# Performance work log

Measured on AMD Instinct MI355X. Metric: run time of the kernel, lower is better.

The kernel has to match this reference:

```python
import jax, jax.numpy as jnp
import numpy as np

B, S, D, H = 128, 1024, 128, 256
ODE_UNFOLDS = 6
EPS = 1e-8


def setup_inputs() -> dict:
    key = jax.random.key(0)
    ks = jax.random.split(key, 14)
    u = lambda k, shape, lo, hi: jax.random.uniform(k, shape, jnp.float32, lo, hi)
    # ncps LTCCell default init ranges; FullyConnected wiring => sparsity masks all ones,
    # erev entries are +/-1 polarities (prob 2/3 excitatory)
    return {
        "x": jax.random.normal(ks[0], (B, S, D), jnp.float32),
        "gleak": u(ks[1], (H,), 0.001, 1.0),
        "vleak": u(ks[2], (H,), -0.2, 0.2),
        "cm": u(ks[3], (H,), 0.4, 0.6),
        "w": u(ks[4], (H, H), 0.001, 1.0),
        "sigma": u(ks[5], (H, H), 3.0, 8.0),
        "mu": u(ks[6], (H, H), 0.3, 0.8),
        "erev": jax.random.bernoulli(ks[7], 2.0 / 3.0, (H, H)).astype(jnp.float32) * 2.0 - 1.0,
        "sensory_w": u(ks[8], (D, H), 0.001, 1.0),
        "sensory_sigma": u(ks[9], (D, H), 3.0, 8.0),
        "sensory_mu": u(ks[10], (D, H), 0.3, 0.8),
        "sensory_erev": jax.random.bernoulli(ks[11], 2.0 / 3.0, (D, H)).astype(jnp.float32) * 2.0 - 1.0,
        "input_w": jnp.ones((D,), jnp.float32),
        "input_b": jnp.zeros((D,), jnp.float32),
    }


def reference(x, gleak, vleak, cm, w, sigma, mu, erev,
              sensory_w, sensory_sigma, sensory_mu, sensory_erev,
              input_w, input_b):
    # NoiseLTC forward in eval mode (noise applied only when training).
    # implicit_param_constraints=True => softplus on gleak, cm, w, sensory_w.
    sp = jax.nn.softplus
    gleak_p = sp(gleak)                      # [H]
    cm_t = sp(cm) * ODE_UNFOLDS             # cm / (elapsed_time=1.0 / ode_unfolds)
    w_p = sp(w)                              # [H, H]
    sw_p = sp(sensory_w)                     # [D, H]

    def step(h, xt):
        xin = xt * input_w + input_b         # affine input mapping, [B, D]
        # sensory synapse activation: [B, D, H]
        s_act = sw_p * jax.nn.sigmoid(sensory_sigma * (xin[:, :, None] - sensory_mu))
        w_num_s = jnp.sum(s_act * sensory_erev, axis=1)  # [B, H]
        w_den_s = jnp.sum(s_act, axis=1)                 # [B, H]

        def unfold(v, _):
            w_act = w_p * jax.nn.sigmoid(sigma * (v[:, :, None] - mu))  # [B, H, H]
            w_num = jnp.sum(w_act * erev, axis=1) + w_num_s
            w_den = jnp.sum(w_act, axis=1) + w_den_s
            num = cm_t * v + gleak_p * vleak + w_num
            den = cm_t + gleak_p + w_den
            return num / (den + EPS), None

        v, _ = jax.lax.scan(unfold, h, None, length=ODE_UNFOLDS)
        # output_size == state_size, so output is the full new state
        return v, v

    h0 = jnp.zeros((x.shape[0], H), x.dtype)
    h_final, outs = jax.lax.scan(step, h0, jnp.swapaxes(x, 0, 1))  # outs: [S, B, H]
    readout = jnp.swapaxes(outs, 0, 1)                             # [B, S, H]
    return readout, h_final
```

## Files before the change

### kernel.cpp

```cpp
#include <hip/hip_runtime.h>
#include <hip/hip_bf16.h>

#define HN 256
#define DN 128
#define SL 1024
#define BN 128
#define NUNF 6

static __device__ __forceinline__ float fexp2(float x) { return __builtin_amdgcn_exp2f(x); }
static __device__ __forceinline__ float frcp(float x) { return __builtin_amdgcn_rcpf(x); }

__global__ void ltc_prep(const float* __restrict__ gleak, const float* __restrict__ vleak,
                         const float* __restrict__ cm,    const float* __restrict__ w,
                         const float* __restrict__ sigma, const float* __restrict__ mu,
                         const float* __restrict__ erev,
                         const float* __restrict__ sw,    const float* __restrict__ ssig,
                         const float* __restrict__ smu,   const float* __restrict__ serev,
                         const float* __restrict__ iw,    const float* __restrict__ ib,
                         float* __restrict__ ws)
{
    const float L2E = 1.44269504088896340736f;
    float* rp  = ws;
    float* spp = ws + 3 * HN * HN;
    float* hv  = ws + 3 * HN * HN + 3 * DN * HN;
    const int stride = gridDim.x * blockDim.x;
    const int tid0 = blockIdx.x * blockDim.x + threadIdx.x;

    for (int idx = tid0; idx < HN * HN; idx += stride) {
        float sg = sigma[idx];
        float wp = log1pf(expf(w[idx]));
        rp[3 * idx + 0] = -sg * L2E;
        rp[3 * idx + 1] = sg * mu[idx] * L2E;
        rp[3 * idx + 2] = wp * erev[idx];
    }
    for (int idx = tid0; idx < DN * HN; idx += stride) {
        int d = idx >> 8;
        float sg = ssig[idx];
        float wp = log1pf(expf(sw[idx]));
        spp[3 * idx + 0] = -sg * L2E * iw[d];
        spp[3 * idx + 1] = sg * (smu[idx] - ib[d]) * L2E;
        spp[3 * idx + 2] = wp * serev[idx];
    }
    if (tid0 < HN) {
        float gl = log1pf(expf(gleak[tid0]));
        float ct = log1pf(expf(cm[tid0])) * (float)NUNF;
        hv[tid0]          = gl * vleak[tid0];
        hv[HN + tid0]     = ct;
        hv[2 * HN + tid0] = ct + gl;
    }
}

__global__ __launch_bounds__(1024) void ltc_main(
    const float* __restrict__ x, const float* __restrict__ rp,
    const float* __restrict__ spp, const float* __restrict__ hv,
    float* __restrict__ out)
{
    const int b = blockIdx.x;
    const int tid = threadIdx.x;
    const int h = tid & (HN - 1);
    const int c = tid >> 8;

    __shared__ __align__(16) float v_[HN];
    __shared__ __align__(16) float xs[DN];
    __shared__ __align__(16) float sred[4][HN][2];

    float cmt = 0.f, gv = 0.f, dcn = 0.f;
    if (tid < HN) {
        gv  = hv[tid];
        cmt = hv[HN + tid];
        dcn = hv[2 * HN + tid];
        v_[tid] = 0.f;
    }
    __syncthreads();

    const float* xrow = x + (size_t)b * SL * DN;
    float* orow = out + (size_t)b * SL * HN;
    float wns = 0.f, wds = 0.f, vnew = 0.f;

    for (int t = 0; t < SL; ++t) {
        if (tid < DN) xs[tid] = xrow[(size_t)t * DN + tid];
        __syncthreads();

        {
            float sn = 0.f, sd = 0.f;
            const float* p = spp + (size_t)(c * 32 * HN + h) * 3;
            const float4* xv4 = reinterpret_cast<const float4*>(&xs[c * 32]);
            #pragma unroll 2
            for (int j = 0; j < 8; ++j) {
                float4 xv = xv4[j];
                #pragma unroll
                for (int q = 0; q < 4; ++q) {
                    float xq = (q == 0) ? xv.x : (q == 1) ? xv.y : (q == 2) ? xv.z : xv.w;
                    float pa = p[0], pb = p[1], pc = p[2];
                    float u = fexp2(fmaf(pa, xq, pb));
                    float r = frcp(1.0f + u);
                    sn = fmaf(pc, r, sn);
                    sd = fmaf(fabsf(pc), r, sd);
                    p += 3 * HN;
                }
            }
            sred[c][h][0] = sn;
            sred[c][h][1] = sd;
        }
        __syncthreads();
        if (tid < HN) {
            wns = sred[0][tid][0] + sred[1][tid][0] + sred[2][tid][0] + sred[3][tid][0];
            wds = sred[0][tid][1] + sred[1][tid][1] + sred[2][tid][1] + sred[3][tid][1];
        }
        __syncthreads();

        #pragma unroll 1
        for (int k = 0; k < NUNF; ++k) {
            float nm = 0.f, dn = 0.f;
            const float* p = rp + (size_t)(c * 64 * HN + h) * 3;
            const float4* v4 = reinterpret_cast<const float4*>(&v_[c * 64]);
            #pragma unroll 2
            for (int j = 0; j < 16; ++j) {
                float4 vv = v4[j];
                #pragma unroll
                for (int q = 0; q < 4; ++q) {
                    float vq = (q == 0) ? vv.x : (q == 1) ? vv.y : (q == 2) ? vv.z : vv.w;
                    float pa = p[0], pb = p[1], pc = p[2];
                    float u = fexp2(fmaf(pa, vq, pb));
                    float r = frcp(1.0f + u);
                    nm = fmaf(pc, r, nm);
                    dn = fmaf(fabsf(pc), r, dn);
                    p += 3 * HN;
                }
            }
            sred[c][h][0] = nm;
            sred[c][h][1] = dn;
            __syncthreads();
            if (tid < HN) {
                float num = sred[0][tid][0] + sred[1][tid][0] + sred[2][tid][0] + sred[3][tid][0] + wns;
                float den = sred[0][tid][1] + sred[1][tid][1] + sred[2][tid][1] + sred[3][tid][1] + wds;
                float vo = v_[tid];
                num = fmaf(cmt, vo, gv) + num;
                den = dcn + den + 1e-8f;
                vnew = num / den;
                v_[tid] = vnew;
            }
            __syncthreads();
        }

        if (tid < HN) orow[(size_t)t * HN + tid] = vnew;
    }
    if (tid < HN) out[(size_t)BN * SL * HN + (size_t)b * HN + tid] = vnew;
}

extern "C" void kernel_launch(void* const* d_in, const int* in_sizes, int n_in,
                              void* d_out, int out_size, void* d_ws, size_t ws_size,
                              hipStream_t stream) {
    const float* x     = (const float*)d_in[0];
    const float* gleak = (const float*)d_in[1];
    const float* vleak = (const float*)d_in[2];
    const float* cm    = (const float*)d_in[3];
    const float* w     = (const float*)d_in[4];
    const float* sigma = (const float*)d_in[5];
    const float* mu    = (const float*)d_in[6];
    const float* erev  = (const float*)d_in[7];
    const float* sw    = (const float*)d_in[8];
    const float* ssig  = (const float*)d_in[9];
    const float* smu   = (const float*)d_in[10];
    const float* serev = (const float*)d_in[11];
    const float* iw    = (const float*)d_in[12];
    const float* ib    = (const float*)d_in[13];

    float* ws = (float*)d_ws;

    ltc_prep<<<128, 256, 0, stream>>>(gleak, vleak, cm, w, sigma, mu, erev,
                                      sw, ssig, smu, serev, iw, ib, ws);

    const float* rp  = ws;
    const float* spp = ws + 3 * HN * HN;
    const float* hv  = ws + 3 * HN * HN + 3 * DN * HN;
    ltc_main<<<BN, 1024, 0, stream>>>(x, rp, spp, hv, (float*)d_out);
}
```

Before: 50.12 ms.

## Pack sigmoid params as fp16 pairs in per-thread contiguous layout with vector loads

After: 95.44 ms. 90.4% more time.

```diff
diff --git a/kernel.cpp b/kernel.cpp
--- a/kernel.cpp
+++ b/kernel.cpp
@@ -1,5 +1,6 @@
 #include <hip/hip_runtime.h>
 #include <hip/hip_bf16.h>
+#include <hip/hip_fp16.h>
 
 #define HN 256
 #define DN 128
@@ -20,26 +21,33 @@
                          float* __restrict__ ws)
 {
     const float L2E = 1.44269504088896340736f;
-    float* rp  = ws;
-    float* spp = ws + 3 * HN * HN;
-    float* hv  = ws + 3 * HN * HN + 3 * DN * HN;
+    float2* rp2  = (float2*)ws;
+    float2* spp2 = (float2*)ws + HN * HN;
+    float*  hv   = ws + 2 * (HN * HN + DN * HN);
     const int stride = gridDim.x * blockDim.x;
     const int tid0 = blockIdx.x * blockDim.x + threadIdx.x;
 
     for (int idx = tid0; idx < HN * HN; idx += stride) {
+        int i = idx >> 8, h = idx & (HN - 1);
         float sg = sigma[idx];
         float wp = log1pf(expf(w[idx]));
-        rp[3 * idx + 0] = -sg * L2E;
-        rp[3 * idx + 1] = sg * mu[idx] * L2E;
-        rp[3 * idx + 2] = wp * erev[idx];
+        unsigned int ua = __half_as_ushort(__float2half_rn(-sg * L2E));
+        unsigned int ub = __half_as_ushort(__float2half_rn(sg * mu[idx] * L2E));
+        float2 e;
+        e.x = __uint_as_float(ua | (ub << 16));
+        e.y = wp * erev[idx];
+        rp2[h * HN + i] = e;
     }
     for (int idx = tid0; idx < DN * HN; idx += stride) {
-        int d = idx >> 8;
+        int d = idx >> 8, h = idx & (HN - 1);
         float sg = ssig[idx];
         float wp = log1pf(expf(sw[idx]));
-        spp[3 * idx + 0] = -sg * L2E * iw[d];
-        spp[3 * idx + 1] = sg * (smu[idx] - ib[d]) * L2E;
-        spp[3 * idx + 2] = wp * serev[idx];
+        unsigned int ua = __half_as_ushort(__float2half_rn(-sg * L2E * iw[d]));
+        unsigned int ub = __half_as_ushort(__float2half_rn(sg * (smu[idx] - ib[d]) * L2E));
+        float2 e;
+        e.x = __uint_as_float(ua | (ub << 16));
+        e.y = wp * serev[idx];
+        spp2[h * DN + d] = e;
     }
     if (tid0 < HN) {
         float gl = log1pf(expf(gleak[tid0]));
@@ -50,9 +58,20 @@
     }
 }
 
+static __device__ __forceinline__ void sig_acc(float px, float py, float v,
+                                               float& nm, float& dn) {
+    __half2 h2 = *reinterpret_cast<const __half2*>(&px);
+    float A = __low2float(h2);
+    float B = __high2float(h2);
+    float e = fexp2(fmaf(A, v, B));
+    float r = frcp(1.0f + e);
+    nm = fmaf(py, r, nm);
+    dn = fmaf(fabsf(py), r, dn);
+}
+
 __global__ __launch_bounds__(1024) void ltc_main(
-    const float* __restrict__ x, const float* __restrict__ rp,
-    const float* __restrict__ spp, const float* __restrict__ hv,
+    const float* __restrict__ x, const float2* __restrict__ rp2,
+    const float2* __restrict__ spp2, const float* __restrict__ hv,
     float* __restrict__ out)
 {
     const int b = blockIdx.x;
@@ -63,6 +82,7 @@
     __shared__ __align__(16) float v_[HN];
     __shared__ __align__(16) float xs[DN];
     __shared__ __align__(16) float sred[4][HN][2];
+    __shared__ __align__(16) float sredS[4][HN][2];
 
     float cmt = 0.f, gv = 0.f, dcn = 0.f;
     if (tid < HN) {
@@ -72,6 +92,9 @@
         v_[tid] = 0.f;
     }
     __syncthreads();
+
+    const float4* rpv = reinterpret_cast<const float4*>(rp2 + (size_t)h * HN + c * 64);
+    const float4* spv = reinterpret_cast<const float4*>(spp2 + (size_t)h * DN + c * 32);
 
     const float* xrow = x + (size_t)b * SL * DN;
     float* orow = out + (size_t)b * SL * HN;
@@ -83,50 +106,47 @@
 
         {
             float sn = 0.f, sd = 0.f;
-            const float* p = spp + (size_t)(c * 32 * HN + h) * 3;
             const float4* xv4 = reinterpret_cast<const float4*>(&xs[c * 32]);
             #pragma unroll 2
-            for (int j = 0; j < 8; ++j) {
-                float4 xv = xv4[j];
-                #pragma unroll
-                for (int q = 0; q < 4; ++q) {
-                    float xq = (q == 0) ? xv.x : (q == 1) ? xv.y : (q == 2) ? xv.z : xv.w;
-                    float pa = p[0], pb = p[1], pc = p[2];
-                    float u = fexp2(fmaf(pa, xq, pb));
-                    float r = frcp(1.0f + u);
-                    sn = fmaf(pc, r, sn);
-                    sd = fmaf(fabsf(pc), r, sd);
-                    p += 3 * HN;
-                }
+            for (int jj = 0; jj < 4; ++jj) {
+                float4 P0 = spv[4 * jj + 0], P1 = spv[4 * jj + 1];
+                float4 P2 = spv[4 * jj + 2], P3 = spv[4 * jj + 3];
+                float4 va = xv4[2 * jj], vb = xv4[2 * jj + 1];
+                sig_acc(P0.x, P0.y, va.x, sn, sd);
+                sig_acc(P0.z, P0.w, va.y, sn, sd);
+                sig_acc(P1.x, P1.y, va.z, sn, sd);
+                sig_acc(P1.z, P1.w, va.w, sn, sd);
+                sig_acc(P2.x, P2.y, vb.x, sn, sd);
+                sig_acc(P2.z, P2.w, vb.y, sn, sd);
+                sig_acc(P3.x, P3.y, vb.z, sn, sd);
+                sig_acc(P3.z, P3.w, vb.w, sn, sd);
             }
-            sred[c][h][0] = sn;
-            sred[c][h][1] = sd;
+            sredS[c][h][0] = sn;
+            sredS[c][h][1] = sd;
         }
         __syncthreads();
         if (tid < HN) {
-            wns = sred[0][tid][0] + sred[1][tid][0] + sred[2][tid][0] + sred[3][tid][0];
-            wds = sred[0][tid][1] + sred[1][tid][1] + sred[2][tid][1] + sred[3][tid][1];
+            wns = sredS[0][tid][0] + sredS[1][tid][0] + sredS[2][tid][0] + sredS[3][tid][0];
+            wds = sredS[0][tid][1] + sredS[1][tid][1] + sredS[2][tid][1] + sredS[3][tid][1];
         }
-        __syncthreads();
 
         #pragma unroll 1
         for (int k = 0; k < NUNF; ++k) {
             float nm = 0.f, dn = 0.f;
-            const float* p = rp + (size_t)(c * 64 * HN + h) * 3;
             const float4* v4 = reinterpret_cast<const float4*>(&v_[c * 64]);
             #pragma unroll 2
-            for (int j = 0; j < 16; ++j) {
-                float4 vv = v4[j];
-                #pragma unroll
-                for (int q = 0; q < 4; ++q) {
-                    float vq = (q == 0) ? vv.x : (q == 1) ? vv.y : (q == 2) ? vv.z : vv.w;
-                    float pa = p[0], pb = p[1], pc = p[2];
-                    float u = fexp2(fmaf(pa, vq, pb));
-                    float r = frcp(1.0f + u);
-                    nm = fmaf(pc, r, nm);
-                    dn = fmaf(fabsf(pc), r, dn);
-                    p += 3 * HN;
-                }
+            for (int jj = 0; jj < 8; ++jj) {
+                float4 P0 = rpv[4 * jj + 0], P1 = rpv[4 * jj + 1];
+                float4 P2 = rpv[4 * jj + 2], P3 = rpv[4 * jj + 3];
+                float4 va = v4[2 * jj], vb = v4[2 * jj + 1];
+                sig_acc(P0.x, P0.y, va.x, nm, dn);
+                sig_acc(P0.z, P0.w, va.y, nm, dn);
+                sig_acc(P1.x, P1.y, va.z, nm, dn);
+                sig_acc(P1.z, P1.w, va.w, nm, dn);
+                sig_acc(P2.x, P2.y, vb.x, nm, dn);
+                sig_acc(P2.z, P2.w, vb.y, nm, dn);
+                sig_acc(P3.x, P3.y, vb.z, nm, dn);
+                sig_acc(P3.z, P3.w, vb.w, nm, dn);
             }
             sred[c][h][0] = nm;
             sred[c][h][1] = dn;
@@ -137,7 +157,7 @@
                 float vo = v_[tid];
                 num = fmaf(cmt, vo, gv) + num;
                 den = dcn + den + 1e-8f;
-                vnew = num / den;
+                vnew = num * frcp(den);
                 v_[tid] = vnew;
             }
             __syncthreads();
@@ -171,8 +191,8 @@
     ltc_prep<<<128, 256, 0, stream>>>(gleak, vleak, cm, w, sigma, mu, erev,
                                       sw, ssig, smu, serev, iw, ib, ws);
 
-    const float* rp  = ws;
-    const float* spp = ws + 3 * HN * HN;
-    const float* hv  = ws + 3 * HN * HN + 3 * DN * HN;
-    ltc_main<<<BN, 1024, 0, stream>>>(x, rp, spp, hv, (float*)d_out);
+    const float2* rp2  = (const float2*)ws;
+    const float2* spp2 = (const float2*)ws + HN * HN;
+    const float*  hv   = ws + 2 * (HN * HN + DN * HN);
+    ltc_main<<<BN, 1024, 0, stream>>>(x, rp2, spp2, hv, (float*)d_out);
 }
```
